# Performance work log

Measured on AMD Instinct MI355X. Metric: run time of the kernel, lower is better.

The kernel has to match this reference:

```python
import jax, jax.numpy as jnp
import numpy as np

N_QUBITS = 16
N_LAYERS = 2
NUM_CLASSES = 10
BATCH = 256

# CNOT as (c_out, t_out, c_in, t_in)
_CNOT = np.zeros((2, 2, 2, 2), dtype=np.complex64)
_CNOT[0, 0, 0, 0] = 1; _CNOT[0, 1, 0, 1] = 1
_CNOT[1, 1, 1, 0] = 1; _CNOT[1, 0, 1, 1] = 1
CNOT = jnp.asarray(_CNOT)


def rot_matrix(phi, theta, omega):
    # PennyLane Rot = RZ(omega) @ RY(theta) @ RZ(phi)
    c, s = jnp.cos(theta / 2), jnp.sin(theta / 2)
    m00 = jnp.exp(-0.5j * (phi + omega)) * c
    m01 = -jnp.exp(0.5j * (phi - omega)) * s
    m10 = jnp.exp(-0.5j * (phi - omega)) * s
    m11 = jnp.exp(0.5j * (phi + omega)) * c
    return jnp.stack([jnp.stack([m00, m01]), jnp.stack([m10, m11])]).astype(jnp.complex64)


def apply_1q(state, U, w, n):
    # state: (B, 2**n); wire 0 = most-significant bit (PennyLane convention)
    B = state.shape[0]
    st = state.reshape(B, 2 ** w, 2, -1)
    st = jnp.einsum('oi,baic->baoc', U, st)
    return st.reshape(B, -1)


def apply_cnot(state, c, t, n):
    B = state.shape[0]
    st = state.reshape((B,) + (2,) * n)
    st = jnp.tensordot(CNOT, st, axes=[[2, 3], [c + 1, t + 1]])  # new c,t axes at front
    st = jnp.moveaxis(st, [0, 1], [c + 1, t + 1])
    return st.reshape(B, -1)


def circuit_expvals(x, q_params, n, n_layers):
    # AmplitudeEmbedding with normalize=True
    norm = jnp.sqrt(jnp.sum(x * x, axis=-1, keepdims=True))
    psi = (x / norm).astype(jnp.complex64)
    for l in range(n_layers):
        for w in range(n):
            U = rot_matrix(q_params[l, w, 0], q_params[l, w, 1], q_params[l, w, 2])
            psi = apply_1q(psi, U, w, n)
        r = (l % (n - 1)) + 1  # default StronglyEntanglingLayers ranges
        for w in range(n):
            psi = apply_cnot(psi, w, (w + r) % n, n)
    probs = psi.real ** 2 + psi.imag ** 2  # (B, 2**n)
    B = probs.shape[0]
    ev = []
    for w in range(n):
        p = probs.reshape(B, 2 ** w, 2, -1)
        ev.append(p[:, :, 0, :].sum(axis=(1, 2)) - p[:, :, 1, :].sum(axis=(1, 2)))
    return jnp.stack(ev, axis=1)  # (B, n)


def setup_inputs() -> dict:
    key = jax.random.key(0)
    k1, k2, k3, k4 = jax.random.split(key, 4)
    x = jax.random.normal(k1, (BATCH, 2 ** N_QUBITS), dtype=jnp.float32)
    q_params = jax.random.normal(k2, (N_LAYERS, N_QUBITS, 3), dtype=jnp.float32)
    lim = 1.0 / np.sqrt(N_QUBITS)
    W = jax.random.uniform(k3, (NUM_CLASSES, N_QUBITS), jnp.float32, -lim, lim)
    b = jax.random.uniform(k4, (NUM_CLASSES,), jnp.float32, -lim, lim)
    return {"x": x, "q_params": q_params, "W": W, "b": b}


def reference(x, q_params, W, b):
    feats = circuit_expvals(x, q_params, N_QUBITS, N_LAYERS)  # (B, n_qubits)
    return feats @ W.T + b
```

## Files before the change

kernel.cpp:

```cpp
#include <hip/hip_runtime.h>


#define BATCH 256
#define NCLS 10

typedef float v2f __attribute__((ext_vector_type(2)));
typedef _Float16 f16x2 __attribute__((ext_vector_type(2)));

struct CircuitMeta { unsigned l1mask[16]; unsigned l1role[16]; unsigned fin[16]; };

__host__ __device__ constexpr CircuitMeta make_meta() {
  CircuitMeta m{};
  unsigned col[16], inv[16];
  for (int w = 0; w < 16; ++w) { col[w] = 1u << (15 - w); inv[w] = 1u << (15 - w); }
  for (int w = 0; w < 16; ++w) { int c = w, t = (w + 1) & 15; col[c] ^= col[t]; inv[t] ^= inv[c]; }
  for (int w = 0; w < 16; ++w) { m.l1mask[w] = col[w]; m.l1role[w] = inv[w]; }
  for (int w = 0; w < 16; ++w) { int c = w, t = (w + 2) & 15; col[c] ^= col[t]; inv[t] ^= inv[c]; }
  for (int w = 0; w < 16; ++w) m.fin[w] = inv[w];
  return m;
}
constexpr CircuitMeta META = make_meta();

__host__ __device__ constexpr unsigned HASH(unsigned i) {
  return i ^ ((i >> 4) & 15u) ^ ((i >> 8) & 15u);
}

__device__ __forceinline__ v2f swp(v2f a) { return __builtin_shufflevector(a, a, 1, 0); }

__device__ __forceinline__ unsigned PK(v2f a) {
  return __builtin_bit_cast(unsigned, __builtin_amdgcn_cvt_pkrtz(a.x, a.y));
}
__device__ __forceinline__ v2f UNPK(unsigned u) {
  f16x2 h = __builtin_bit_cast(f16x2, u);
  return (v2f){(float)h.x, (float)h.y};
}

template<int B0,int B1,int B2,int B3,int B4>
__host__ __device__ constexpr unsigned regval5(int j) {
  return ((unsigned)(j & 1) << B0) | ((unsigned)((j >> 1) & 1) << B1) |
         ((unsigned)((j >> 2) & 1) << B2) | ((unsigned)((j >> 3) & 1) << B3) |
         ((unsigned)((j >> 4) & 1) << B4);
}

template<int B0,int B1,int B2,int B3,int B4, unsigned MG, unsigned RG>
__device__ __forceinline__ void gate5(v2f (&A)[32], const float* __restrict__ g,
                                      int gi, unsigned tp) {
  constexpr unsigned cover = (1u<<B0)|(1u<<B1)|(1u<<B2)|(1u<<B3)|(1u<<B4);
  static_assert((MG & ~cover) == 0u, "gate mask not covered by stage reg bits");
  constexpr unsigned mr = ((MG>>B0)&1u) | (((MG>>B1)&1u)<<1) | (((MG>>B2)&1u)<<2)
                        | (((MG>>B3)&1u)<<3) | (((MG>>B4)&1u)<<4);
  static_assert(mr != 0u, "empty reg mask");
  constexpr unsigned pivot = mr & (0u - mr);

  float u00r = g[gi*8+0], u00i = g[gi*8+1], u01r = g[gi*8+2], u01i = g[gi*8+3];
  float u10r = g[gi*8+4], u10i = g[gi*8+5], u11r = g[gi*8+6], u11i = g[gi*8+7];
  const bool s = (__popc(RG & tp) & 1) != 0;
  float e00r = s ? u11r : u00r, e00i = s ? u11i : u00i;
  float e01r = s ? u10r : u01r, e01i = s ? u10i : u01i;
  float e10r = s ? u01r : u10r, e10i = s ? u01i : u10i;
  float e11r = s ? u00r : u11r, e11i = s ? u00i : u11i;
  v2f a00 = {e00r, e00r}, b00 = {-e00i, e00i};
  v2f a01 = {e01r, e01r}, b01 = {-e01i, e01i};
  v2f a10 = {e10r, e10r}, b10 = {-e10i, e10i};
  v2f a11 = {e11r, e11r}, b11 = {-e11i, e11i};

  #pragma unroll
  for (int j0 = 0; j0 < 32; ++j0) {
    if (j0 & (int)pivot) continue;
    const int j1 = j0 ^ (int)mr;
    const bool podd =
      (__builtin_popcount(RG & regval5<B0,B1,B2,B3,B4>(j0)) & 1) != 0;
    v2f v0 = A[j0], v1 = A[j1];
    v2f v0s = swp(v0), v1s = swp(v1);
    if (!podd) {
      A[j0] = a00*v0 + b00*v0s + a01*v1 + b01*v1s;
      A[j1] = a10*v0 + b10*v0s + a11*v1 + b11*v1s;
    } else {
      A[j0] = a11*v0 + b11*v0s + a10*v1 + b10*v1s;
      A[j1] = a01*v0 + b01*v0s + a00*v1 + b00*v1s;
    }
  }
}

__global__ void prep_gates(const float* __restrict__ qp, float* __restrict__ g) {
  int i = threadIdx.x;
  if (i >= 32) return;
  float phi = qp[i*3+0], th = qp[i*3+1], om = qp[i*3+2];
  float cth = cosf(0.5f*th), sth = sinf(0.5f*th);
  float a = 0.5f*(phi+om), d = 0.5f*(phi-om);
  float ca = cosf(a), sa = sinf(a), cd = cosf(d), sd = sinf(d);
  g[i*8+0] =  ca*cth; g[i*8+1] = -sa*cth;
  g[i*8+2] = -cd*sth; g[i*8+3] = -sd*sth;
  g[i*8+4] =  cd*sth; g[i*8+5] = -sd*sth;
  g[i*8+6] =  ca*cth; g[i*8+7] =  sa*cth;
}

__global__ __launch_bounds__(256, 4) void passA(const float* __restrict__ x,
    unsigned* __restrict__ st, const float* __restrict__ g) {
  __shared__ unsigned L[8192];
  const int t = threadIdx.x;
  const int batch = blockIdx.x >> 3;
  const unsigned f = blockIdx.x & 7;
  const float* xb = x + ((size_t)batch << 16) + ((size_t)f << 13);

  v2f A[32];
  #pragma unroll
  for (int j = 0; j < 32; ++j) A[j] = (v2f){xb[((unsigned)j << 8) | (unsigned)t], 0.f};

  gate5<8,9,10,11,12, 0x1000u,0x1000u>(A, g, 3, 0u);
  gate5<8,9,10,11,12, 0x0800u,0x0800u>(A, g, 4, 0u);
  gate5<8,9,10,11,12, 0x0400u,0x0400u>(A, g, 5, 0u);
  gate5<8,9,10,11,12, 0x0200u,0x0200u>(A, g, 6, 0u);
  gate5<8,9,10,11,12, 0x0100u,0x0100u>(A, g, 7, 0u);

  {
    const unsigned wb = HASH((unsigned)t);
    #pragma unroll
    for (int j = 0; j < 32; ++j) L[wb ^ HASH((unsigned)j << 8)] = PK(A[j]);
    __syncthreads();
    const unsigned rb = HASH((((unsigned)t & 0xF8u) << 5) | ((unsigned)t & 7u));
    #pragma unroll
    for (int j = 0; j < 32; ++j) A[j] = UNPK(L[rb ^ HASH((unsigned)j << 3)]);
  }

  gate5<3,4,5,6,7, 0x0080u,0x0080u>(A, g,  8, 0u);
  gate5<3,4,5,6,7, 0x0040u,0x0040u>(A, g,  9, 0u);
  gate5<3,4,5,6,7, 0x0020u,0x0020u>(A, g, 10, 0u);
  gate5<3,4,5,6,7, 0x0010u,0x0010u>(A, g, 11, 0u);
  gate5<3,4,5,6,7, 0x0008u,0x0008u>(A, g, 12, 0u);

  __syncthreads();
  {
    const unsigned wb = HASH((((unsigned)t & 0xF8u) << 5) | ((unsigned)t & 7u));
    #pragma unroll
    for (int j = 0; j < 32; ++j) L[wb ^ HASH((unsigned)j << 3)] = PK(A[j]);
    __syncthreads();
    const unsigned rb = HASH((unsigned)t << 3);
    #pragma unroll
    for (int j = 0; j < 32; ++j)
      A[j] = UNPK(L[rb ^ HASH(((unsigned)j & 7u) | (((unsigned)j & 24u) << 8))]);
  }

  gate5<0,1,2,11,12, 0x0004u,0x0004u>(A, g, 13, 0u);
  gate5<0,1,2,11,12, 0x0002u,0x0002u>(A, g, 14, 0u);
  gate5<0,1,2,11,12, 0x0001u,0x0001u>(A, g, 15, 0u);

  unsigned* outb = st + ((size_t)batch << 16) + ((size_t)f << 13);
  #pragma unroll
  for (int jh = 0; jh < 4; ++jh) {
    uint4 q0, q1;
    q0.x = PK(A[jh*8+0]); q0.y = PK(A[jh*8+1]); q0.z = PK(A[jh*8+2]); q0.w = PK(A[jh*8+3]);
    q1.x = PK(A[jh*8+4]); q1.y = PK(A[jh*8+5]); q1.z = PK(A[jh*8+6]); q1.w = PK(A[jh*8+7]);
    const unsigned si = ((unsigned)jh << 11) | ((unsigned)t << 3);
    *(uint4*)(outb + si) = q0;
    *(uint4*)(outb + si + 4) = q1;
  }
}

__global__ __launch_bounds__(256, 4) void passB(unsigned* __restrict__ st,
    const float* __restrict__ g) {
  __shared__ unsigned L[8192];
  const int t = threadIdx.x;
  const int batch = blockIdx.x >> 3;
  const unsigned c = blockIdx.x & 7;
  unsigned* stb = st + ((size_t)batch << 16);

  const unsigned lbase = ((unsigned)t & 127u) | (((unsigned)t & 128u) << 3) | (c << 7);
  v2f A[32];
  #pragma unroll
  for (int j = 0; j < 32; ++j) A[j] = UNPK(stb[((unsigned)j << 11) | lbase]);

  const unsigned tp1 = lbase;
  gate5<11,12,13,14,15, 0x8000u,0x8000u>(A, g, 0, tp1);
  gate5<11,12,13,14,15, 0x4000u,0x4000u>(A, g, 1, tp1);
  gate5<11,12,13,14,15, 0x2000u,0x2000u>(A, g, 2, tp1);
  gate5<11,12,13,14,15, META.l1mask[0], META.l1role[0]>(A, g, 16, tp1);
  gate5<11,12,13,14,15, META.l1mask[1], META.l1role[1]>(A, g, 17, tp1);
  gate5<11,12,13,14,15, META.l1mask[2], META.l1role[2]>(A, g, 18, tp1);
  gate5<11,12,13,14,15, META.l1mask[3], META.l1role[3]>(A, g, 19, tp1);

  {
    const unsigned wb = HASH((unsigned)t);
    #pragma unroll
    for (int j = 0; j < 32; ++j) L[wb ^ HASH((unsigned)j << 8)] = PK(A[j]);
    __syncthreads();
    const unsigned rb = HASH((((unsigned)t & 0xF0u) << 5) | (((unsigned)t & 15u) << 1));
    #pragma unroll
    for (int j = 0; j < 32; ++j)
      A[j] = UNPK(L[rb ^ HASH(((unsigned)j & 1u) | (((unsigned)j & 30u) << 4))]);
  }

  const unsigned tp2 = (((unsigned)t & 0xF0u) << 8) | (((unsigned)t & 15u) << 1) | (c << 7);
  gate5<0,5,6,10,11, META.l1mask[4], META.l1role[4]>(A, g, 20, tp2);
  gate5<0,5,6,10,11, META.l1mask[9], META.l1role[9]>(A, g, 25, tp2);

  __syncthreads();
  {
    const unsigned wb = HASH((((unsigned)t & 0xF0u) << 5) | (((unsigned)t & 15u) << 1));
    #pragma unroll
    for (int j = 0; j < 32; ++j)
      L[wb ^ HASH(((unsigned)j & 1u) | (((unsigned)j & 30u) << 4))] = PK(A[j]);
    __syncthreads();
    const unsigned rb = HASH((((unsigned)t & 0xFEu) << 5) | ((unsigned)t & 1u));
    #pragma unroll
    for (int j = 0; j < 32; ++j) A[j] = UNPK(L[rb ^ HASH((unsigned)j << 1)]);
  }

  const unsigned tp3 = (((unsigned)t & 0xFCu) << 8) | (((unsigned)t & 2u) << 5)
                     | ((unsigned)t & 1u) | (c << 7);
  gate5<1,2,3,4,5, META.l1mask[10], META.l1role[10]>(A, g, 26, tp3);
  gate5<1,2,3,4,5, META.l1mask[11], META.l1role[11]>(A, g, 27, tp3);
  gate5<1,2,3,4,5, META.l1mask[12], META.l1role[12]>(A, g, 28, tp3);
  gate5<1,2,3,4,5, META.l1mask[13], META.l1role[13]>(A, g, 29, tp3);

  __syncthreads();
  {
    const unsigned wb = HASH((((unsigned)t & 0xFEu) << 5) | ((unsigned)t & 1u));
    #pragma unroll
    for (int j = 0; j < 32; ++j) L[wb ^ HASH((unsigned)j << 1)] = PK(A[j]);
    __syncthreads();
    const unsigned rb = HASH((unsigned)t << 2);
    #pragma unroll
    for (int j = 0; j < 32; ++j)
      A[j] = UNPK(L[rb ^ HASH(((unsigned)j & 3u) | (((unsigned)j & 28u) << 8))]);
  }

  const unsigned tp4 = (((unsigned)t & 0xE0u) << 5) | (((unsigned)t & 31u) << 2) | (c << 7);
  gate5<0,1,13,14,15, META.l1mask[14], META.l1role[14]>(A, g, 30, tp4);
  gate5<0,1,13,14,15, META.l1mask[15], META.l1role[15]>(A, g, 31, tp4);

  #pragma unroll
  for (int jh = 0; jh < 8; ++jh) {
    uint4 q;
    q.x = PK(A[jh*4+0]); q.y = PK(A[jh*4+1]); q.z = PK(A[jh*4+2]); q.w = PK(A[jh*4+3]);
    *(uint4*)(stb + (tp4 | ((unsigned)jh << 13))) = q;
  }
}

__global__ __launch_bounds__(256, 4) void passC(const unsigned* __restrict__ st,
    const float* __restrict__ g, float* __restrict__ partials) {
  __shared__ float R[4][17];
  const int t = threadIdx.x;
  const int batch = blockIdx.x >> 3;
  const unsigned f = blockIdx.x & 7;
  const unsigned* stb = st + ((size_t)batch << 16);

  const unsigned cbase = (f << 13) | (((unsigned)t & 192u) << 5) | ((unsigned)t & 63u);
  v2f A[32];
  #pragma unroll
  for (int j = 0; j < 32; ++j) A[j] = UNPK(stb[cbase | ((unsigned)j << 6)]);

  gate5<6,7,8,9,10, META.l1mask[5], META.l1role[5]>(A, g, 21, cbase);
  gate5<6,7,8,9,10, META.l1mask[6], META.l1role[6]>(A, g, 22, cbase);
  gate5<6,7,8,9,10, META.l1mask[7], META.l1role[7]>(A, g, 23, cbase);
  gate5<6,7,8,9,10, META.l1mask[8], META.l1role[8]>(A, g, 24, cbase);

  float sv[16], tot = 0.f;
  #pragma unroll
  for (int w = 0; w < 16; ++w) sv[w] = 0.f;
  #pragma unroll
  for (int j = 0; j < 32; ++j) {
    const float pr = A[j].x*A[j].x + A[j].y*A[j].y;
    tot += pr;
    #pragma unroll
    for (int w = 0; w < 16; ++w) {
      const bool neg = (__builtin_popcount(META.fin[w] & ((unsigned)j << 6)) & 1) != 0;
      sv[w] += neg ? -pr : pr;
    }
  }
  #pragma unroll
  for (int w = 0; w < 16; ++w)
    if (__popc(META.fin[w] & cbase) & 1) sv[w] = -sv[w];

  #pragma unroll
  for (int off = 32; off; off >>= 1) {
    tot += __shfl_xor(tot, off, 64);
    #pragma unroll
    for (int w = 0; w < 16; ++w) sv[w] += __shfl_xor(sv[w], off, 64);
  }
  const int wave = t >> 6, lane = t & 63;
  if (lane == 0) {
    #pragma unroll
    for (int w = 0; w < 16; ++w) R[wave][w] = sv[w];
    R[wave][16] = tot;
  }
  __syncthreads();
  if (t < 17) {
    const float s2 = R[0][t] + R[1][t] + R[2][t] + R[3][t];
    partials[(size_t)blockIdx.x * 17 + t] = s2;
  }
}

__global__ __launch_bounds__(64) void head(const float* __restrict__ partials,
    const float* __restrict__ W, const float* __restrict__ bias,
    float* __restrict__ out) {
  const int b = blockIdx.x, tid = threadIdx.x;
  __shared__ float red[17];
  __shared__ float ev[16];
  if (tid < 17) {
    float s = 0.f;
    #pragma unroll
    for (int ch = 0; ch < 8; ++ch) s += partials[(size_t)((b << 3) + ch) * 17 + tid];
    red[tid] = s;
  }
  __syncthreads();
  if (tid < 16) ev[tid] = red[tid] / red[16];
  __syncthreads();
  if (tid < NCLS) {
    float o = bias[tid];
    #pragma unroll
    for (int w = 0; w < 16; ++w) o += ev[w] * W[tid*16 + w];
    out[b*NCLS + tid] = o;
  }
}

extern "C" void kernel_launch(void* const* d_in, const int* in_sizes, int n_in,
                              void* d_out, int out_size, void* d_ws, size_t ws_size,
                              hipStream_t stream) {
  const float* x  = (const float*)d_in[0];
  const float* qp = (const float*)d_in[1];
  const float* W  = (const float*)d_in[2];
  const float* bv = (const float*)d_in[3];
  float* out = (float*)d_out;

  unsigned* st     = (unsigned*)d_ws;
  float*    gates  = (float*)((char*)d_ws + (size_t)BATCH * 65536 * 4);
  float*    parts  = (float*)((char*)gates + 1024);

  prep_gates<<<dim3(1), dim3(64), 0, stream>>>(qp, gates);
  passA<<<dim3(BATCH*8), dim3(256), 0, stream>>>(x, st, gates);
  passB<<<dim3(BATCH*8), dim3(256), 0, stream>>>(st, gates);
  passC<<<dim3(BATCH*8), dim3(256), 0, stream>>>(st, gates, parts);
  head<<<dim3(BATCH), dim3(64), 0, stream>>>(parts, W, bv, out);
}
```

Before: 197.8 us.

## Halve per-thread amplitudes with 512-thread blocks and re-plan gate stages in passA/passB

passA and passB now run 512 threads per block, each holding 16 amplitudes instead of 32, with a new 4-bit gate4 helper. The gate order and LDS transpose stages are re-planned to match. Global loads become vectorized float4/uint2 reads, and the LDS swizzle hash gains an extra term. The aim is to cut register pressure and raise occupancy and memory parallelism, at the cost of one more shared-memory transpose round and a changed passB output layout that passC must still read correctly.

```diff
diff --git a/kernel.cpp b/kernel.cpp
--- a/kernel.cpp
+++ b/kernel.cpp
@@ -21,12 +21,14 @@
 }
 constexpr CircuitMeta META = make_meta();
 
-__host__ __device__ constexpr unsigned HASH(unsigned i) {
-  return i ^ ((i >> 4) & 15u) ^ ((i >> 8) & 15u);
+__host__ __device__ constexpr unsigned HSH(unsigned p) {
+  return p ^ ((p >> 4) & 15u) ^ ((p >> 8) & 15u) ^ ((p >> 5) & 3u);
+}
+__host__ __device__ constexpr unsigned GIDX(unsigned p) {
+  return (p & 0x7Fu) | ((p & 0x1F80u) << 3);
 }
 
 __device__ __forceinline__ v2f swp(v2f a) { return __builtin_shufflevector(a, a, 1, 0); }
-
 __device__ __forceinline__ unsigned PK(v2f a) {
   return __builtin_bit_cast(unsigned, __builtin_amdgcn_cvt_pkrtz(a.x, a.y));
 }
@@ -35,11 +37,54 @@
   return (v2f){(float)h.x, (float)h.y};
 }
 
+template<int B0,int B1,int B2,int B3>
+__host__ __device__ constexpr unsigned regval4(int j) {
+  return ((unsigned)(j & 1) << B0) | ((unsigned)((j >> 1) & 1) << B1) |
+         ((unsigned)((j >> 2) & 1) << B2) | ((unsigned)((j >> 3) & 1) << B3);
+}
 template<int B0,int B1,int B2,int B3,int B4>
 __host__ __device__ constexpr unsigned regval5(int j) {
-  return ((unsigned)(j & 1) << B0) | ((unsigned)((j >> 1) & 1) << B1) |
-         ((unsigned)((j >> 2) & 1) << B2) | ((unsigned)((j >> 3) & 1) << B3) |
-         ((unsigned)((j >> 4) & 1) << B4);
+  return regval4<B0,B1,B2,B3>(j) | ((unsigned)((j >> 4) & 1) << B4);
+}
+
+template<int B0,int B1,int B2,int B3, unsigned MG, unsigned RG>
+__device__ __forceinline__ void gate4(v2f (&A)[16], const float* __restrict__ g,
+                                      int gi, unsigned tp) {
+  constexpr unsigned cover = (1u<<B0)|(1u<<B1)|(1u<<B2)|(1u<<B3);
+  static_assert((MG & ~cover) == 0u, "gate mask not covered by stage reg bits");
+  constexpr unsigned mr = ((MG>>B0)&1u) | (((MG>>B1)&1u)<<1) | (((MG>>B2)&1u)<<2)
+                        | (((MG>>B3)&1u)<<3);
+  static_assert(mr != 0u, "empty reg mask");
+  constexpr unsigned pivot = mr & (0u - mr);
+
+  float u00r = g[gi*8+0], u00i = g[gi*8+1], u01r = g[gi*8+2], u01i = g[gi*8+3];
+  float u10r = g[gi*8+4], u10i = g[gi*8+5], u11r = g[gi*8+6], u11i = g[gi*8+7];
+  const bool s = (__popc(RG & tp) & 1) != 0;
+  float e00r = s ? u11r : u00r, e00i = s ? u11i : u00i;
+  float e01r = s ? u10r : u01r, e01i = s ? u10i : u01i;
+  float e10r = s ? u01r : u10r, e10i = s ? u01i : u10i;
+  float e11r = s ? u00r : u11r, e11i = s ? u00i : u11i;
+  v2f a00 = {e00r, e00r}, b00 = {-e00i, e00i};
+  v2f a01 = {e01r, e01r}, b01 = {-e01i, e01i};
+  v2f a10 = {e10r, e10r}, b10 = {-e10i, e10i};
+  v2f a11 = {e11r, e11r}, b11 = {-e11i, e11i};
+
+  #pragma unroll
+  for (int j0 = 0; j0 < 16; ++j0) {
+    if (j0 & (int)pivot) continue;
+    const int j1 = j0 ^ (int)mr;
+    const bool podd =
+      (__builtin_popcount(RG & regval4<B0,B1,B2,B3>(j0)) & 1) != 0;
+    v2f v0 = A[j0], v1 = A[j1];
+    v2f v0s = swp(v0), v1s = swp(v1);
+    if (!podd) {
+      A[j0] = a00*v0 + b00*v0s + a01*v1 + b01*v1s;
+      A[j1] = a10*v0 + b10*v0s + a11*v1 + b11*v1s;
+    } else {
+      A[j0] = a11*v0 + b11*v0s + a10*v1 + b10*v1s;
+      A[j1] = a01*v0 + b01*v0s + a00*v1 + b00*v1s;
+    }
+  }
 }
 
 template<int B0,int B1,int B2,int B3,int B4, unsigned MG, unsigned RG>
@@ -95,145 +140,163 @@
   g[i*8+6] =  ca*cth; g[i*8+7] =  sa*cth;
 }
 
-__global__ __launch_bounds__(256, 4) void passA(const float* __restrict__ x,
+__global__ __launch_bounds__(512, 6) void passA(const float* __restrict__ x,
     unsigned* __restrict__ st, const float* __restrict__ g) {
   __shared__ unsigned L[8192];
   const int t = threadIdx.x;
   const int batch = blockIdx.x >> 3;
   const unsigned f = blockIdx.x & 7;
-  const float* xb = x + ((size_t)batch << 16) + ((size_t)f << 13);
-
-  v2f A[32];
-  #pragma unroll
-  for (int j = 0; j < 32; ++j) A[j] = (v2f){xb[((unsigned)j << 8) | (unsigned)t], 0.f};
-
-  gate5<8,9,10,11,12, 0x1000u,0x1000u>(A, g, 3, 0u);
-  gate5<8,9,10,11,12, 0x0800u,0x0800u>(A, g, 4, 0u);
-  gate5<8,9,10,11,12, 0x0400u,0x0400u>(A, g, 5, 0u);
-  gate5<8,9,10,11,12, 0x0200u,0x0200u>(A, g, 6, 0u);
-  gate5<8,9,10,11,12, 0x0100u,0x0100u>(A, g, 7, 0u);
-
-  {
-    const unsigned wb = HASH((unsigned)t);
-    #pragma unroll
-    for (int j = 0; j < 32; ++j) L[wb ^ HASH((unsigned)j << 8)] = PK(A[j]);
-    __syncthreads();
-    const unsigned rb = HASH((((unsigned)t & 0xF8u) << 5) | ((unsigned)t & 7u));
-    #pragma unroll
-    for (int j = 0; j < 32; ++j) A[j] = UNPK(L[rb ^ HASH((unsigned)j << 3)]);
-  }
-
-  gate5<3,4,5,6,7, 0x0080u,0x0080u>(A, g,  8, 0u);
-  gate5<3,4,5,6,7, 0x0040u,0x0040u>(A, g,  9, 0u);
-  gate5<3,4,5,6,7, 0x0020u,0x0020u>(A, g, 10, 0u);
-  gate5<3,4,5,6,7, 0x0010u,0x0010u>(A, g, 11, 0u);
-  gate5<3,4,5,6,7, 0x0008u,0x0008u>(A, g, 12, 0u);
-
-  __syncthreads();
-  {
-    const unsigned wb = HASH((((unsigned)t & 0xF8u) << 5) | ((unsigned)t & 7u));
-    #pragma unroll
-    for (int j = 0; j < 32; ++j) L[wb ^ HASH((unsigned)j << 3)] = PK(A[j]);
-    __syncthreads();
-    const unsigned rb = HASH((unsigned)t << 3);
-    #pragma unroll
-    for (int j = 0; j < 32; ++j)
-      A[j] = UNPK(L[rb ^ HASH(((unsigned)j & 7u) | (((unsigned)j & 24u) << 8))]);
-  }
-
-  gate5<0,1,2,11,12, 0x0004u,0x0004u>(A, g, 13, 0u);
-  gate5<0,1,2,11,12, 0x0002u,0x0002u>(A, g, 14, 0u);
-  gate5<0,1,2,11,12, 0x0001u,0x0001u>(A, g, 15, 0u);
-
-  unsigned* outb = st + ((size_t)batch << 16) + ((size_t)f << 13);
+  const float4* xb4 = (const float4*)(x + ((size_t)batch << 16) + ((size_t)f << 13));
+
+  v2f A[16];
   #pragma unroll
   for (int jh = 0; jh < 4; ++jh) {
+    float4 v = xb4[(unsigned)t | ((unsigned)jh << 9)];
+    A[jh*4+0] = (v2f){v.x, 0.f}; A[jh*4+1] = (v2f){v.y, 0.f};
+    A[jh*4+2] = (v2f){v.z, 0.f}; A[jh*4+3] = (v2f){v.w, 0.f};
+  }
+
+  gate4<0,1,11,12, 0x0001u,0x0001u>(A, g, 15, 0u);
+  gate4<0,1,11,12, 0x0002u,0x0002u>(A, g, 14, 0u);
+  gate4<0,1,11,12, 0x0800u,0x0800u>(A, g,  4, 0u);
+  gate4<0,1,11,12, 0x1000u,0x1000u>(A, g,  3, 0u);
+
+  {
+    const unsigned wb = HSH((unsigned)t << 2);
+    #pragma unroll
+    for (int j = 0; j < 16; ++j)
+      L[wb ^ HSH(((unsigned)j & 3u) | (((unsigned)j & 12u) << 9))] = PK(A[j]);
+    __syncthreads();
+    const unsigned rb = HSH(((unsigned)t & 0x7Fu) | (((unsigned)t & 0x180u) << 4));
+    #pragma unroll
+    for (int j = 0; j < 16; ++j) A[j] = UNPK(L[rb ^ HSH((unsigned)j << 7)]);
+  }
+
+  gate4<7,8,9,10, 0x0080u,0x0080u>(A, g, 8, 0u);
+  gate4<7,8,9,10, 0x0100u,0x0100u>(A, g, 7, 0u);
+  gate4<7,8,9,10, 0x0200u,0x0200u>(A, g, 6, 0u);
+  gate4<7,8,9,10, 0x0400u,0x0400u>(A, g, 5, 0u);
+
+  __syncthreads();
+  {
+    const unsigned wb = HSH(((unsigned)t & 0x7Fu) | (((unsigned)t & 0x180u) << 4));
+    #pragma unroll
+    for (int j = 0; j < 16; ++j) L[wb ^ HSH((unsigned)j << 7)] = PK(A[j]);
+    __syncthreads();
+    const unsigned rb = HSH(((unsigned)t & 7u) | (((unsigned)t & 0x1F8u) << 4));
+    #pragma unroll
+    for (int j = 0; j < 16; ++j) A[j] = UNPK(L[rb ^ HSH((unsigned)j << 3)]);
+  }
+
+  gate4<3,4,5,6, 0x0008u,0x0008u>(A, g, 12, 0u);
+  gate4<3,4,5,6, 0x0010u,0x0010u>(A, g, 11, 0u);
+  gate4<3,4,5,6, 0x0020u,0x0020u>(A, g, 10, 0u);
+  gate4<3,4,5,6, 0x0040u,0x0040u>(A, g,  9, 0u);
+
+  __syncthreads();
+  {
+    const unsigned wb = HSH(((unsigned)t & 7u) | (((unsigned)t & 0x1F8u) << 4));
+    #pragma unroll
+    for (int j = 0; j < 16; ++j) L[wb ^ HSH((unsigned)j << 3)] = PK(A[j]);
+    __syncthreads();
+    const unsigned rb = HSH((unsigned)t << 3);
+    #pragma unroll
+    for (int j = 0; j < 16; ++j)
+      A[j] = UNPK(L[rb ^ HSH(((unsigned)j & 7u) | (((unsigned)j & 8u) << 9))]);
+  }
+
+  gate4<0,1,2,12, 0x0004u,0x0004u>(A, g, 13, 0u);
+
+  unsigned* outb = st + ((size_t)batch << 16) + ((size_t)f << 13) + ((size_t)t << 3);
+  #pragma unroll
+  for (int h = 0; h < 2; ++h) {
     uint4 q0, q1;
-    q0.x = PK(A[jh*8+0]); q0.y = PK(A[jh*8+1]); q0.z = PK(A[jh*8+2]); q0.w = PK(A[jh*8+3]);
-    q1.x = PK(A[jh*8+4]); q1.y = PK(A[jh*8+5]); q1.z = PK(A[jh*8+6]); q1.w = PK(A[jh*8+7]);
-    const unsigned si = ((unsigned)jh << 11) | ((unsigned)t << 3);
-    *(uint4*)(outb + si) = q0;
-    *(uint4*)(outb + si + 4) = q1;
-  }
-}
-
-__global__ __launch_bounds__(256, 4) void passB(unsigned* __restrict__ st,
+    q0.x = PK(A[h*8+0]); q0.y = PK(A[h*8+1]); q0.z = PK(A[h*8+2]); q0.w = PK(A[h*8+3]);
+    q1.x = PK(A[h*8+4]); q1.y = PK(A[h*8+5]); q1.z = PK(A[h*8+6]); q1.w = PK(A[h*8+7]);
+    *(uint4*)(outb + h*4096 + 0) = q0;
+    *(uint4*)(outb + h*4096 + 4) = q1;
+  }
+}
+
+__global__ __launch_bounds__(512, 6) void passB(unsigned* __restrict__ st,
     const float* __restrict__ g) {
   __shared__ unsigned L[8192];
   const int t = threadIdx.x;
   const int batch = blockIdx.x >> 3;
-  const unsigned c = blockIdx.x & 7;
+  const unsigned c7 = (blockIdx.x & 7u) << 7;
   unsigned* stb = st + ((size_t)batch << 16);
 
-  const unsigned lbase = ((unsigned)t & 127u) | (((unsigned)t & 128u) << 3) | (c << 7);
-  v2f A[32];
-  #pragma unroll
-  for (int j = 0; j < 32; ++j) A[j] = UNPK(stb[((unsigned)j << 11) | lbase]);
-
-  const unsigned tp1 = lbase;
-  gate5<11,12,13,14,15, 0x8000u,0x8000u>(A, g, 0, tp1);
-  gate5<11,12,13,14,15, 0x4000u,0x4000u>(A, g, 1, tp1);
-  gate5<11,12,13,14,15, 0x2000u,0x2000u>(A, g, 2, tp1);
-  gate5<11,12,13,14,15, META.l1mask[0], META.l1role[0]>(A, g, 16, tp1);
-  gate5<11,12,13,14,15, META.l1mask[1], META.l1role[1]>(A, g, 17, tp1);
-  gate5<11,12,13,14,15, META.l1mask[2], META.l1role[2]>(A, g, 18, tp1);
-  gate5<11,12,13,14,15, META.l1mask[3], META.l1role[3]>(A, g, 19, tp1);
-
-  {
-    const unsigned wb = HASH((unsigned)t);
-    #pragma unroll
-    for (int j = 0; j < 32; ++j) L[wb ^ HASH((unsigned)j << 8)] = PK(A[j]);
-    __syncthreads();
-    const unsigned rb = HASH((((unsigned)t & 0xF0u) << 5) | (((unsigned)t & 15u) << 1));
-    #pragma unroll
-    for (int j = 0; j < 32; ++j)
-      A[j] = UNPK(L[rb ^ HASH(((unsigned)j & 1u) | (((unsigned)j & 30u) << 4))]);
-  }
-
-  const unsigned tp2 = (((unsigned)t & 0xF0u) << 8) | (((unsigned)t & 15u) << 1) | (c << 7);
-  gate5<0,5,6,10,11, META.l1mask[4], META.l1role[4]>(A, g, 20, tp2);
-  gate5<0,5,6,10,11, META.l1mask[9], META.l1role[9]>(A, g, 25, tp2);
-
-  __syncthreads();
-  {
-    const unsigned wb = HASH((((unsigned)t & 0xF0u) << 5) | (((unsigned)t & 15u) << 1));
-    #pragma unroll
-    for (int j = 0; j < 32; ++j)
-      L[wb ^ HASH(((unsigned)j & 1u) | (((unsigned)j & 30u) << 4))] = PK(A[j]);
-    __syncthreads();
-    const unsigned rb = HASH((((unsigned)t & 0xFEu) << 5) | ((unsigned)t & 1u));
-    #pragma unroll
-    for (int j = 0; j < 32; ++j) A[j] = UNPK(L[rb ^ HASH((unsigned)j << 1)]);
-  }
-
-  const unsigned tp3 = (((unsigned)t & 0xFCu) << 8) | (((unsigned)t & 2u) << 5)
-                     | ((unsigned)t & 1u) | (c << 7);
-  gate5<1,2,3,4,5, META.l1mask[10], META.l1role[10]>(A, g, 26, tp3);
-  gate5<1,2,3,4,5, META.l1mask[11], META.l1role[11]>(A, g, 27, tp3);
-  gate5<1,2,3,4,5, META.l1mask[12], META.l1role[12]>(A, g, 28, tp3);
-  gate5<1,2,3,4,5, META.l1mask[13], META.l1role[13]>(A, g, 29, tp3);
-
-  __syncthreads();
-  {
-    const unsigned wb = HASH((((unsigned)t & 0xFEu) << 5) | ((unsigned)t & 1u));
-    #pragma unroll
-    for (int j = 0; j < 32; ++j) L[wb ^ HASH((unsigned)j << 1)] = PK(A[j]);
-    __syncthreads();
-    const unsigned rb = HASH((unsigned)t << 2);
-    #pragma unroll
-    for (int j = 0; j < 32; ++j)
-      A[j] = UNPK(L[rb ^ HASH(((unsigned)j & 3u) | (((unsigned)j & 28u) << 8))]);
-  }
-
-  const unsigned tp4 = (((unsigned)t & 0xE0u) << 5) | (((unsigned)t & 31u) << 2) | (c << 7);
-  gate5<0,1,13,14,15, META.l1mask[14], META.l1role[14]>(A, g, 30, tp4);
-  gate5<0,1,13,14,15, META.l1mask[15], META.l1role[15]>(A, g, 31, tp4);
-
-  #pragma unroll
-  for (int jh = 0; jh < 8; ++jh) {
-    uint4 q;
-    q.x = PK(A[jh*4+0]); q.y = PK(A[jh*4+1]); q.z = PK(A[jh*4+2]); q.w = PK(A[jh*4+3]);
-    *(uint4*)(stb + (tp4 | ((unsigned)jh << 13))) = q;
+  v2f A[16];
+  #pragma unroll
+  for (int jp = 0; jp < 8; ++jp) {
+    const unsigned p = ((unsigned)t << 1) | ((unsigned)jp << 10);
+    const uint2 u = *(const uint2*)(stb + (GIDX(p) | c7));
+    A[2*jp]   = UNPK(u.x);
+    A[2*jp+1] = UNPK(u.y);
+  }
+
+  const unsigned tp1 = GIDX((unsigned)t << 1) | c7;
+  gate4<0,13,14,15, 0x8000u,0x8000u>(A, g, 0, tp1);
+  gate4<0,13,14,15, 0x4000u,0x4000u>(A, g, 1, tp1);
+  gate4<0,13,14,15, 0x2000u,0x2000u>(A, g, 2, tp1);
+  gate4<0,13,14,15, META.l1mask[0],  META.l1role[0]> (A, g, 16, tp1);
+  gate4<0,13,14,15, META.l1mask[1],  META.l1role[1]> (A, g, 17, tp1);
+  gate4<0,13,14,15, META.l1mask[15], META.l1role[15]>(A, g, 31, tp1);
+
+  {
+    const unsigned wb = HSH((unsigned)t << 1);
+    #pragma unroll
+    for (int j = 0; j < 16; ++j)
+      L[wb ^ HSH(((unsigned)j & 1u) | (((unsigned)j & 14u) << 9))] = PK(A[j]);
+    __syncthreads();
+    const unsigned rb = HSH(((unsigned)t & 0x7Fu) | (((unsigned)t & 0x180u) << 4));
+    #pragma unroll
+    for (int j = 0; j < 16; ++j) A[j] = UNPK(L[rb ^ HSH((unsigned)j << 7)]);
+  }
+
+  const unsigned tp2 = GIDX(((unsigned)t & 0x7Fu) | (((unsigned)t & 0x180u) << 4)) | c7;
+  gate4<10,11,12,13, META.l1mask[2], META.l1role[2]>(A, g, 18, tp2);
+  gate4<10,11,12,13, META.l1mask[3], META.l1role[3]>(A, g, 19, tp2);
+  gate4<10,11,12,13, META.l1mask[4], META.l1role[4]>(A, g, 20, tp2);
+
+  __syncthreads();
+  {
+    const unsigned wb = HSH(((unsigned)t & 0x7Fu) | (((unsigned)t & 0x180u) << 4));
+    #pragma unroll
+    for (int j = 0; j < 16; ++j) L[wb ^ HSH((unsigned)j << 7)] = PK(A[j]);
+    __syncthreads();
+    const unsigned rb = HSH(((unsigned)t & 7u) | (((unsigned)t & 0x1F8u) << 4));
+    #pragma unroll
+    for (int j = 0; j < 16; ++j) A[j] = UNPK(L[rb ^ HSH((unsigned)j << 3)]);
+  }
+
+  const unsigned tp3 = GIDX(((unsigned)t & 7u) | (((unsigned)t & 0x1F8u) << 4)) | c7;
+  gate4<3,4,5,6, META.l1mask[9],  META.l1role[9]> (A, g, 25, tp3);
+  gate4<3,4,5,6, META.l1mask[10], META.l1role[10]>(A, g, 26, tp3);
+  gate4<3,4,5,6, META.l1mask[11], META.l1role[11]>(A, g, 27, tp3);
+
+  __syncthreads();
+  {
+    const unsigned wb = HSH(((unsigned)t & 7u) | (((unsigned)t & 0x1F8u) << 4));
+    #pragma unroll
+    for (int j = 0; j < 16; ++j) L[wb ^ HSH((unsigned)j << 3)] = PK(A[j]);
+    __syncthreads();
+    const unsigned rb = HSH((unsigned)t << 4);
+    #pragma unroll
+    for (int j = 0; j < 16; ++j) A[j] = UNPK(L[rb ^ HSH((unsigned)j)]);
+  }
+
+  const unsigned tp4 = GIDX((unsigned)t << 4) | c7;
+  gate4<0,1,2,3, META.l1mask[12], META.l1role[12]>(A, g, 28, tp4);
+  gate4<0,1,2,3, META.l1mask[13], META.l1role[13]>(A, g, 29, tp4);
+  gate4<0,1,2,3, META.l1mask[14], META.l1role[14]>(A, g, 30, tp4);
+
+  unsigned* outb = stb + (GIDX((unsigned)t << 4) | c7);
+  #pragma unroll
+  for (int q = 0; q < 4; ++q) {
+    uint4 v;
+    v.x = PK(A[q*4+0]); v.y = PK(A[q*4+1]); v.z = PK(A[q*4+2]); v.w = PK(A[q*4+3]);
+    *(uint4*)(outb + q*4) = v;
   }
 }
 
@@ -328,8 +391,8 @@
   float*    parts  = (float*)((char*)gates + 1024);
 
   prep_gates<<<dim3(1), dim3(64), 0, stream>>>(qp, gates);
-  passA<<<dim3(BATCH*8), dim3(256), 0, stream>>>(x, st, gates);
-  passB<<<dim3(BATCH*8), dim3(256), 0, stream>>>(st, gates);
+  passA<<<dim3(BATCH*8), dim3(512), 0, stream>>>(x, st, gates);
+  passB<<<dim3(BATCH*8), dim3(512), 0, stream>>>(st, gates);
   passC<<<dim3(BATCH*8), dim3(256), 0, stream>>>(st, gates, parts);
   head<<<dim3(BATCH), dim3(64), 0, stream>>>(parts, W, bv, out);
 }
```

Result: slower. 211.6 us (+7.0%).
